# Kernel optimization log

Measured on AMD Instinct MI355X. Metric: run time of the kernel, lower is better.

## Reference

```python
import jax, jax.numpy as jnp
import numpy as np

B, L = 1, 2048
D_MODEL, N_LAYER, D_INNER = 768, 2, 1536
D_STATE, DT_RANK, D_CONV, OUT_DIM = 16, 48, 4, 128


def setup_inputs() -> dict:
    key = jax.random.key(0)
    ks = jax.random.split(key, 10)
    s = 0.02
    p = {}
    p["x"] = jax.random.normal(ks[0], (B, L, D_MODEL), jnp.float32)
    # stacked per-layer parameters, leading dim = N_LAYER
    p["in_proj_w"] = jax.random.normal(ks[1], (N_LAYER, 2 * D_INNER, D_MODEL), jnp.float32) * s
    p["conv_w"] = jax.random.normal(ks[2], (N_LAYER, D_INNER, D_CONV), jnp.float32) * s
    p["conv_b"] = jnp.zeros((N_LAYER, D_INNER), jnp.float32)
    p["x_proj_w"] = jax.random.normal(ks[3], (N_LAYER, DT_RANK + 2 * D_STATE, D_INNER), jnp.float32) * s
    p["dt_proj_w"] = jax.random.normal(ks[4], (N_LAYER, D_INNER, DT_RANK), jnp.float32) * s
    p["dt_proj_b"] = jax.random.normal(ks[5], (N_LAYER, D_INNER), jnp.float32) * s
    A = jnp.tile(jnp.arange(1, D_STATE + 1, dtype=jnp.float32)[None, :], (D_INNER, 1))
    p["A_log"] = jnp.tile(jnp.log(A)[None], (N_LAYER, 1, 1))
    p["D"] = jnp.ones((N_LAYER, D_INNER), jnp.float32)
    p["out_proj_w"] = jax.random.normal(ks[6], (N_LAYER, D_MODEL, D_INNER), jnp.float32) * s
    p["norm_w"] = jnp.ones((N_LAYER, D_MODEL), jnp.float32)
    p["norm_f_w"] = jnp.ones((D_MODEL,), jnp.float32)
    p["head_w"] = jax.random.normal(ks[7], (OUT_DIM, D_MODEL), jnp.float32) * s
    return p


def rmsnorm(x, w, eps=1e-5):
    return x * jax.lax.rsqrt(jnp.mean(x * x, -1, keepdims=True) + eps) * w


def selective_scan(u, delta, A, Bm, Cm, Dv):
    # u, delta: (b,l,d); A: (d,n); Bm, Cm: (b,l,n); Dv: (d,)
    dA = jnp.exp(jnp.einsum('bld,dn->bldn', delta, A))       # discretized A
    dBu = jnp.einsum('bld,bln->bldn', delta * u, Bm)          # discretized B*u

    def step(s, inp):
        dA_t, dBu_t, C_t = inp                               # (b,d,n),(b,d,n),(b,n)
        s = dA_t * s + dBu_t
        y = jnp.einsum('bdn,bn->bd', s, C_t)
        return s, y

    s0 = jnp.zeros((u.shape[0], u.shape[2], A.shape[1]), u.dtype)
    _, ys = jax.lax.scan(step, s0, (dA.transpose(1, 0, 2, 3), dBu.transpose(1, 0, 2, 3), Cm.transpose(1, 0, 2)))
    y = ys.transpose(1, 0, 2)                                # (b,l,d)
    return y + u * Dv


def mamba_block(x, w):
    xr = jnp.einsum('bld,ed->ble', x, w['in_proj_w'])        # (b,l,2*d_inner)
    xin, res = jnp.split(xr, 2, axis=-1)
    # causal depthwise conv1d
    xc = jax.lax.conv_general_dilated(
        xin.transpose(0, 2, 1), w['conv_w'][:, None, :],
        window_strides=(1,), padding=[(D_CONV - 1, 0)],
        dimension_numbers=('NCH', 'OIH', 'NCH'),
        feature_group_count=D_INNER)
    xc = (xc + w['conv_b'][None, :, None]).transpose(0, 2, 1)
    xc = jax.nn.silu(xc)
    # SSM
    A = -jnp.exp(w['A_log'])                                 # (d_inner, d_state)
    proj = jnp.einsum('bld,ed->ble', xc, w['x_proj_w'])
    delta, Bm, Cm = jnp.split(proj, [DT_RANK, DT_RANK + D_STATE], axis=-1)
    delta = jax.nn.softplus(jnp.einsum('blr,dr->bld', delta, w['dt_proj_w']) + w['dt_proj_b'])
    y = selective_scan(xc, delta, A, Bm, Cm, w['D'])
    y = y * jax.nn.silu(res)
    return jnp.einsum('bld,ed->ble', y, w['out_proj_w'])


def reference(x, in_proj_w, conv_w, conv_b, x_proj_w, dt_proj_w, dt_proj_b,
              A_log, D, out_proj_w, norm_w, norm_f_w, head_w):
    stacked = dict(in_proj_w=in_proj_w, conv_w=conv_w, conv_b=conv_b,
                   x_proj_w=x_proj_w, dt_proj_w=dt_proj_w, dt_proj_b=dt_proj_b,
                   A_log=A_log, D=D, out_proj_w=out_proj_w)
    for i in range(N_LAYER):
        w = {k: v[i] for k, v in stacked.items()}
        x = x + mamba_block(rmsnorm(x, norm_w[i]), w)        # pre-norm residual block
    x = rmsnorm(x, norm_f_w)
    return jnp.einsum('bld,od->blo', x, head_w)              # lm_head (no bias)
```

## Files before the change

### kernel.cpp

```cpp
#include <hip/hip_runtime.h>
#include <hip/hip_bf16.h>
#include <stdint.h>

#define LSEQ 2048
#define DM 768
#define DI 1536
#define NCH 128
#define CHK 16

typedef __bf16 bf16;
typedef short short8 __attribute__((ext_vector_type(8)));
typedef float floatx4 __attribute__((ext_vector_type(4)));
typedef bf16 bf16x8 __attribute__((ext_vector_type(8)));

__device__ inline float silu_f(float x){ return x / (1.f + __expf(-x)); }

__device__ __forceinline__ void g2l16(const bf16* g, bf16* l){
  __builtin_amdgcn_global_load_lds(
      (const __attribute__((address_space(1))) void*)g,
      (__attribute__((address_space(3))) void*)l, 16, 0, 0);
}

__device__ inline int bf16_flag(const void* dvv){
  return (*(const unsigned*)dvv == 0x3F803F80u) ? 1 : 0;
}

__device__ inline float ldin(const void* p, long i, int f){
  return f ? (float)((const bf16*)p)[i] : ((const float*)p)[i];
}

__device__ __forceinline__ void ld8(const void* src, long i, int f, float* o){
  if(f){
    bf16x8 v = *(const bf16x8*)((const bf16*)src + i);
    #pragma unroll
    for(int k = 0; k < 8; k++) o[k] = (float)v[k];
  } else {
    float4 a = ((const float4*)src)[i >> 2];
    float4 b = ((const float4*)src)[(i >> 2) + 1];
    o[0]=a.x; o[1]=a.y; o[2]=a.z; o[3]=a.w; o[4]=b.x; o[5]=b.y; o[6]=b.z; o[7]=b.w;
  }
}
__device__ __forceinline__ void st8_bf(bf16* dst, long i, const float* o){
  bf16x8 v;
  #pragma unroll
  for(int k = 0; k < 8; k++) v[k] = (bf16)o[k];
  *(bf16x8*)(dst + i) = v;
}
__device__ __forceinline__ void st8_f32(float* dst, long i, const float* o){
  ((float4*)dst)[i >> 2]       = make_float4(o[0], o[1], o[2], o[3]);
  ((float4*)dst)[(i >> 2) + 1] = make_float4(o[4], o[5], o[6], o[7]);
}

#define NB_INW  2304
#define NB_OUTW 1152
#define NB_HW   48
#define NB_X    768
#define NB_ALOG 24
#define NB_XPW  192
#define NB_DTW  96
#define NB_SM   12
#define NB_TOT  (NB_INW+NB_OUTW+NB_HW+NB_X+NB_ALOG+NB_XPW+NB_DTW+NB_SM)

__global__ __launch_bounds__(256) void k_canon(const void* x_, const void* inw_,
    const void* cw_, const void* cb_, const void* xpw_, const void* dtw_,
    const void* dtb_, const void* dvv_, const void* alog_, const void* outw_,
    const void* nw_, const void* nfw_, const void* hw_,
    float* x0, bf16* inw, float* cw, float* cb, bf16* xpw, bf16* dtw, float* dtb,
    float* alog, float* dv, bf16* outw, float* nw, float* nfw, bf16* hw){
  int f = bf16_flag(dvv_);
  int b = blockIdx.x;
  int t = threadIdx.x;
  float o[8];
  if(b < NB_INW + NB_OUTW + NB_HW){
    const void* src; bf16* dst; long off;
    if(b < NB_INW){ src = inw_; dst = inw; off = (long)b*2048; }
    else if(b < NB_INW + NB_OUTW){ src = outw_; dst = outw; off = (long)(b - NB_INW)*2048; }
    else { src = hw_; dst = hw; off = (long)(b - NB_INW - NB_OUTW)*2048; }
    long i = off + t*8;
    if(f){ *(bf16x8*)(dst + i) = *(const bf16x8*)((const bf16*)src + i); }
    else { ld8(src, i, 0, o); st8_bf(dst, i, o); }
    return;
  }
  b -= NB_INW + NB_OUTW + NB_HW;
  if(b < NB_X + NB_ALOG){
    const void* src; float* dst; long off;
    if(b < NB_X){ src = x_; dst = x0; off = (long)b*2048; }
    else { src = alog_; dst = alog; off = (long)(b - NB_X)*2048; }
    long i = off + t*8;
    ld8(src, i, f, o);
    st8_f32(dst, i, o);
    return;
  }
  b -= NB_X + NB_ALOG;
  if(b < NB_XPW){
    long j = (long)b*2048 + t*8;
    int layer = (int)(j / (128*DI));
    int rem = (int)(j % (128*DI));
    int r = rem / DI, c = rem % DI;
    if(r < 80){
      ld8(xpw_, ((long)layer*80 + r)*DI + c, f, o);
    } else {
      for(int k = 0; k < 8; k++) o[k] = 0.f;
    }
    st8_bf(xpw, j, o);
    return;
  }
  b -= NB_XPW;
  if(b < NB_DTW){
    long j = (long)b*2048 + t*8;
    int layer = (int)(j / (DI*64));
    int rem = (int)(j % (DI*64));
    int r = rem / 64, c = rem % 64;
    if(c < 48){
      ld8(dtw_, ((long)layer*DI + r)*48 + c, f, o);
    } else {
      for(int k = 0; k < 8; k++) o[k] = 0.f;
    }
    st8_bf(dtw, j, o);
    return;
  }
  b -= NB_DTW;
  for(int idx = b*256 + t; idx < 23808; idx += NB_SM*256){
    int j = idx;
    if(j < 12288){ cw[j] = ldin(cw_, j, f); continue; } j -= 12288;
    if(j < 3072){ cb[j] = ldin(cb_, j, f); continue; } j -= 3072;
    if(j < 3072){ dtb[j] = ldin(dtb_, j, f); continue; } j -= 3072;
    if(j < 3072){ dv[j] = ldin(dvv_, j, f); continue; } j -= 3072;
    if(j < 1536){ nw[j] = ldin(nw_, j, f); continue; } j -= 1536;
    nfw[j] = ldin(nfw_, j, f);
  }
}

__global__ __launch_bounds__(256) void k_rmsnorm(const float* __restrict__ x,
    const float* __restrict__ w, bf16* __restrict__ out){
  int row = blockIdx.x;
  const float* xr = x + row*DM;
  int t = threadIdx.x;
  float v0 = xr[t], v1 = xr[t+256], v2 = xr[t+512];
  float ss = v0*v0 + v1*v1 + v2*v2;
  #pragma unroll
  for(int o = 32; o; o >>= 1) ss += __shfl_down(ss, o, 64);
  __shared__ float red[4];
  int lane = t & 63, wid = t >> 6;
  if(lane == 0) red[wid] = ss;
  __syncthreads();
  ss = red[0] + red[1] + red[2] + red[3];
  float rs = rsqrtf(ss / DM + 1e-5f);
  out[row*DM + t]       = (bf16)(v0 * rs * w[t]);
  out[row*DM + t + 256] = (bf16)(v1 * rs * w[t+256]);
  out[row*DM + t + 512] = (bf16)(v2 * rs * w[t+512]);
}

template<int SPLITK, int MODE>
__global__ __launch_bounds__(256) void k_gemm(
    const bf16* __restrict__ A, const bf16* __restrict__ B, void* Cv,
    int K, int ldc, const float* __restrict__ aux){
  __shared__ bf16 sA[64*32];
  __shared__ bf16 sB[128*32];
  int bm0 = blockIdx.y*64, bn0 = blockIdx.x*128;
  int tid = threadIdx.x;
  int lane = tid & 63, wid = tid >> 6;
  int wn = wid*32;
  int quad = lane >> 4, lr = lane & 15;
  const int klen = K / SPLITK;
  const int kbeg = (SPLITK > 1) ? blockIdx.z * klen : 0;
  const bf16* Ag = A + (size_t)(bm0 + (tid>>2))*K + kbeg + (tid&3)*8;
  const bf16* Bg = B + (size_t)(bn0 + (tid>>2))*K + kbeg + (tid&3)*8;
  floatx4 acc[4][2] = {};
  for(int k0 = 0; k0 < klen; k0 += 32){
    __syncthreads();
    g2l16(Ag, sA + tid*8);
    g2l16(Bg, sB + tid*8);
    g2l16(Bg + 64*K, sB + 2048 + tid*8);
    __syncthreads();
    short8 af[4], bf_[2];
    #pragma unroll
    for(int i = 0; i < 4; i++)
      af[i]  = *(const short8*)(sA + (i*16 + lr)*32 + quad*8);
    #pragma unroll
    for(int j = 0; j < 2; j++)
      bf_[j] = *(const short8*)(sB + (wn + j*16 + lr)*32 + quad*8);
    #pragma unroll
    for(int i = 0; i < 4; i++)
      #pragma unroll
      for(int j = 0; j < 2; j++)
        acc[i][j] = __builtin_amdgcn_mfma_f32_16x16x32_bf16(af[i], bf_[j], acc[i][j], 0, 0, 0);
    Ag += 32; Bg += 32;
  }
  float* Cf = (float*)Cv + ((MODE == 5) ? (size_t)blockIdx.z * LSEQ * ldc : 0);
  bf16* Cb = (bf16*)Cv;
  #pragma unroll
  for(int i = 0; i < 4; i++){
    #pragma unroll
    for(int j = 0; j < 2; j++){
      #pragma unroll
      for(int r = 0; r < 4; r++){
        int grow = bm0 + i*16 + quad*4 + r;
        int gcol = bn0 + wn + j*16 + lr;
        float v = acc[i][j][r];
        if(MODE == 0){
          Cb[(size_t)grow*ldc + gcol] = (bf16)v;
        } else if(MODE == 1){
          v += aux[gcol];
          v = fmaxf(v, 0.f) + log1pf(__expf(-fabsf(v)));
          Cb[(size_t)grow*ldc + gcol] = (bf16)v;
        } else {
          Cf[(size_t)grow*ldc + gcol] = v;
        }
      }
    }
  }
  (void)aux;
}

__global__ __launch_bounds__(256) void k_epi_xproj(const float* __restrict__ part,
    float* __restrict__ proj, bf16* __restrict__ dtin){
  int idx = blockIdx.x*256 + threadIdx.x;
  float s = 0.f;
  #pragma unroll
  for(int z = 0; z < 8; z++) s += part[(size_t)z*LSEQ*128 + idx];
  int row = idx >> 7, col = idx & 127;
  if(col < 80) proj[row*80 + col] = s;
  if(col < 64) dtin[row*64 + col] = (col < 48) ? (bf16)s : (bf16)0.f;
}

__global__ __launch_bounds__(256) void k_epi_out_norm(const float* __restrict__ part,
    const float* __restrict__ resid, const float* __restrict__ w,
    float* __restrict__ xws, bf16* __restrict__ xn){
  int row = blockIdx.x;
  int t = threadIdx.x;
  float v[3]; float ss = 0.f;
  #pragma unroll
  for(int k = 0; k < 3; k++){
    long i = (long)row*DM + t + k*256;
    float s = part[i] + part[(long)LSEQ*DM + i] + resid[i];
    xws[i] = s; v[k] = s; ss += s*s;
  }
  #pragma unroll
  for(int o = 32; o; o >>= 1) ss += __shfl_down(ss, o, 64);
  __shared__ float red[4];
  if((t & 63) == 0) red[t >> 6] = ss;
  __syncthreads();
  ss = red[0] + red[1] + red[2] + red[3];
  float rs = rsqrtf(ss / DM + 1e-5f);
  #pragma unroll
  for(int k = 0; k < 3; k++){
    int col = t + k*256;
    xn[(long)row*DM + col] = (bf16)(v[k] * rs * w[col]);
  }
}

__global__ __launch_bounds__(256) void k_epi_head(const float* __restrict__ part,
    const void* dvv, void* out){
  int idx = blockIdx.x*256 + threadIdx.x;
  const int N = LSEQ*128;
  float s = part[idx] + part[N+idx] + part[2*N+idx] + part[3*N+idx];
  if(bf16_flag(dvv)) ((bf16*)out)[idx] = (bf16)s;
  else               ((float*)out)[idx] = s;
}

__global__ __launch_bounds__(256) void k_conv(const bf16* __restrict__ xr,
    const float* __restrict__ cw, const float* __restrict__ cb,
    bf16* __restrict__ xcb){
  int d = blockIdx.x*256 + threadIdx.x;
  int l0 = blockIdx.y*16;
  float w0 = cw[d*4+0], w1 = cw[d*4+1], w2 = cw[d*4+2], w3 = cw[d*4+3];
  float bias = cb[d];
  float xm3 = (l0 >= 3) ? (float)xr[(l0-3)*(2*DI) + d] : 0.f;
  float xm2 = (l0 >= 2) ? (float)xr[(l0-2)*(2*DI) + d] : 0.f;
  float xm1 = (l0 >= 1) ? (float)xr[(l0-1)*(2*DI) + d] : 0.f;
  #pragma unroll
  for(int tl = 0; tl < 16; tl++){
    int l = l0 + tl;
    float xc = (float)xr[l*(2*DI) + d];
    float acc = bias + xm3*w0 + xm2*w1 + xm1*w2 + xc*w3;
    xcb[l*DI + d] = (bf16)silu_f(acc);
    xm3 = xm2; xm2 = xm1; xm1 = xc;
  }
}

__global__ __launch_bounds__(256) void k_scan1(
    const bf16* __restrict__ delta, const bf16* __restrict__ u,
    const float* __restrict__ proj, const float* __restrict__ alog,
    float* __restrict__ Aprod, float* __restrict__ Bsum){
  int d = blockIdx.y*256 + threadIdx.x;
  int c = blockIdx.x;
  __shared__ float Bl[CHK*16];
  {
    int t = threadIdx.x >> 4, n = threadIdx.x & 15;
    Bl[threadIdx.x] = proj[(c*CHK + t)*80 + 48 + n];
  }
  __syncthreads();
  const float L2E = 1.44269504f;
  float An2[16], ap[16], s[16];
  #pragma unroll
  for(int n = 0; n < 16; n++){ An2[n] = -__expf(alog[d*16+n]) * L2E; ap[n] = 1.f; s[n] = 0.f; }
  int t0 = c*CHK;
  float dt = (float)delta[t0*DI + d];
  float uu = (float)u[t0*DI + d];
  #pragma unroll
  for(int tl = 0; tl < CHK; tl++){
    float dtn = 0.f, un = 0.f;
    if(tl + 1 < CHK){
      dtn = (float)delta[(t0+tl+1)*DI + d];
      un = (float)u[(t0+tl+1)*DI + d];
    }
    float du = dt * uu;
    #pragma unroll
    for(int n = 0; n < 16; n++){
      float e = exp2f(dt * An2[n]);
      s[n] = e*s[n] + du*Bl[tl*16+n];
      ap[n] *= e;
    }
    dt = dtn; uu = un;
  }
  int base = (c*DI + d)*16;
  #pragma unroll
  for(int n = 0; n < 16; n++){ Aprod[base+n] = ap[n]; Bsum[base+n] = s[n]; }
}

__global__ __launch_bounds__(256) void k_scan2(const float* __restrict__ Aprod,
    const float* __restrict__ Bsum, float* __restrict__ Sinit){
  int idx = blockIdx.x*256 + threadIdx.x;
  const int STR = DI*16;
  float s = 0.f;
  for(int c0 = 0; c0 < NCH; c0 += 8){
    float a[8], b[8];
    #pragma unroll
    for(int j = 0; j < 8; j++){
      a[j] = Aprod[(size_t)(c0+j)*STR + idx];
      b[j] = Bsum [(size_t)(c0+j)*STR + idx];
    }
    #pragma unroll
    for(int j = 0; j < 8; j++){
      Sinit[(size_t)(c0+j)*STR + idx] = s;
      s = a[j]*s + b[j];
    }
  }
}

__global__ __launch_bounds__(256) void k_scan3(
    const bf16* __restrict__ delta, const bf16* __restrict__ u,
    const float* __restrict__ proj, const float* __restrict__ alog,
    const float* __restrict__ dvp, const float* __restrict__ Sinit,
    const bf16* __restrict__ xr, bf16* __restrict__ ybar){
  int d = blockIdx.y*256 + threadIdx.x;
  int c = blockIdx.x;
  __shared__ float Bl[CHK*16], Cl[CHK*16];
  {
    int t = threadIdx.x >> 4, n = threadIdx.x & 15;
    Bl[threadIdx.x] = proj[(c*CHK + t)*80 + 48 + n];
    Cl[threadIdx.x] = proj[(c*CHK + t)*80 + 64 + n];
  }
  __syncthreads();
  const float L2E = 1.44269504f;
  float An2[16], s[16];
  #pragma unroll
  for(int n = 0; n < 16; n++) An2[n] = -__expf(alog[d*16+n]) * L2E;
  int base = (c*DI + d)*16;
  #pragma unroll
  for(int n = 0; n < 16; n++) s[n] = Sinit[base+n];
  float Dd = dvp[d];
  int t0 = c*CHK;
  float dt = (float)delta[t0*DI + d];
  float uu = (float)u[t0*DI + d];
  float res = (float)xr[t0*(2*DI) + DI + d];
  #pragma unroll
  for(int tl = 0; tl < CHK; tl++){
    float dtn = 0.f, un = 0.f, rn = 0.f;
    if(tl + 1 < CHK){
      dtn = (float)delta[(t0+tl+1)*DI + d];
      un = (float)u[(t0+tl+1)*DI + d];
      rn = (float)xr[(t0+tl+1)*(2*DI) + DI + d];
    }
    float du = dt * uu;
    float y = 0.f;
    #pragma unroll
    for(int n = 0; n < 16; n++){
      float e = exp2f(dt * An2[n]);
      s[n] = e*s[n] + du*Bl[tl*16+n];
      y += s[n]*Cl[tl*16+n];
    }
    y += uu * Dd;
    ybar[(t0+tl)*DI + d] = (bf16)(y * silu_f(res));
    dt = dtn; uu = un; res = rn;
  }
}

extern "C" void kernel_launch(void* const* d_in, const int* in_sizes, int n_in,
                              void* d_out, int out_size, void* d_ws, size_t ws_size,
                              hipStream_t stream){
  const void* x_   = d_in[0];
  const void* inw_ = d_in[1];
  const void* cw_  = d_in[2];
  const void* cb_  = d_in[3];
  const void* xpw_ = d_in[4];
  const void* dtw_ = d_in[5];
  const void* dtb_ = d_in[6];
  const void* alog_= d_in[7];
  const void* dvv_ = d_in[8];
  const void* outw_= d_in[9];
  const void* nw_  = d_in[10];
  const void* nfw_ = d_in[11];
  const void* hw_  = d_in[12];

  char* p = (char*)d_ws;
  auto alloc = [&](size_t n){ char* r = p; p += (n + 255) & ~(size_t)255; return r; };
  float* x0  = (float*)alloc((size_t)LSEQ*DM*4);
  bf16* inw  = (bf16*)alloc((size_t)2*2*DI*DM*2);
  float* cw  = (float*)alloc((size_t)2*DI*4*4);
  float* cb  = (float*)alloc((size_t)2*DI*4);
  bf16* xpw  = (bf16*)alloc((size_t)2*128*DI*2);
  bf16* dtw  = (bf16*)alloc((size_t)2*DI*64*2);
  float* dtb = (float*)alloc((size_t)2*DI*4);
  float* alog= (float*)alloc((size_t)2*DI*16*4);
  float* dv  = (float*)alloc((size_t)2*DI*4);
  bf16* outw = (bf16*)alloc((size_t)2*DM*DI*2);
  float* nw  = (float*)alloc((size_t)2*DM*4);
  float* nfw = (float*)alloc((size_t)DM*4);
  bf16* hw   = (bf16*)alloc((size_t)128*DM*2);
  bf16* xn   = (bf16*)alloc((size_t)LSEQ*DM*2);
  bf16* xr   = (bf16*)alloc((size_t)LSEQ*2*DI*2);
  bf16* xcb  = (bf16*)alloc((size_t)LSEQ*DI*2);
  float* proj= (float*)alloc((size_t)LSEQ*80*4);
  bf16* dtin = (bf16*)alloc((size_t)LSEQ*64*2);
  bf16* delta= (bf16*)alloc((size_t)LSEQ*DI*2);
  float* Aprod=(float*)alloc((size_t)NCH*DI*16*4);
  float* Bsum =(float*)alloc((size_t)NCH*DI*16*4);
  bf16* ybar = (bf16*)alloc((size_t)LSEQ*DI*2);
  float* xws = (float*)alloc((size_t)LSEQ*DM*4);
  float* part = (float*)alloc((size_t)2*LSEQ*DM*4);
  float* Sinit = part;

  k_canon<<<NB_TOT, 256, 0, stream>>>(x_, inw_, cw_, cb_, xpw_, dtw_, dtb_, dvv_,
      alog_, outw_, nw_, nfw_, hw_,
      x0, inw, cw, cb, xpw, dtw, dtb, alog, dv, outw, nw, nfw, hw);

  k_rmsnorm<<<LSEQ, 256, 0, stream>>>(x0, nw, xn);
  const float* xcur = x0;
  for(int i = 0; i < 2; i++){
    k_gemm<1,0><<<dim3(2*DI/128, LSEQ/64), 256, 0, stream>>>(
        xn, inw + (size_t)i*2*DI*DM, xr, DM, 2*DI, nullptr);
    k_conv<<<dim3(DI/256, LSEQ/16), 256, 0, stream>>>(xr, cw + i*DI*4, cb + i*DI, xcb);
    k_gemm<8,5><<<dim3(1, LSEQ/64, 8), 256, 0, stream>>>(
        xcb, xpw + (size_t)i*128*DI, part, DI, 128, nullptr);
    k_epi_xproj<<<LSEQ*128/256, 256, 0, stream>>>(part, proj, dtin);
    k_gemm<1,1><<<dim3(DI/128, LSEQ/64), 256, 0, stream>>>(
        dtin, dtw + (size_t)i*DI*64, delta, 64, DI, dtb + i*DI);
    k_scan1<<<dim3(NCH, DI/256), 256, 0, stream>>>(delta, xcb, proj, alog + i*DI*16, Aprod, Bsum);
    k_scan2<<<DI*16/256, 256, 0, stream>>>(Aprod, Bsum, Sinit);
    k_scan3<<<dim3(NCH, DI/256), 256, 0, stream>>>(delta, xcb, proj, alog + i*DI*16,
        dv + i*DI, Sinit, xr, ybar);
    k_gemm<2,5><<<dim3(DM/128, LSEQ/64, 2), 256, 0, stream>>>(
        ybar, outw + (size_t)i*DM*DI, part, DI, DM, nullptr);
    k_epi_out_norm<<<LSEQ, 256, 0, stream>>>(part, xcur,
        (i == 0) ? (nw + DM) : nfw, xws, xn);
    xcur = xws;
  }
  k_gemm<4,5><<<dim3(1, LSEQ/64, 4), 256, 0, stream>>>(
      xn, hw, part, DM, 128, nullptr);
  k_epi_head<<<LSEQ*128/256, 256, 0, stream>>>(part, dvv_, d_out);

  (void)in_sizes; (void)n_in; (void)out_size; (void)ws_size;
}
```

Baseline: 408.2 us.

## Fuse x_proj split-K reduction with dt_proj softplus; preload scan inputs

Replaces the x_proj epilogue kernel and the separate MFMA dt_proj GEMM with one kernel per row. It reduces the split-K partials, keeps the 48-wide dt row in shared memory, computes dt_proj with scalar FMAs and softplus, and writes delta. This removes one launch and the dtin round trip, but moves the small K=48 GEMM from matrix cores onto vector ALUs. Separately, the scan kernels now load all 16 delta and u values for a chunk up front rather than prefetching one step ahead, which raises register use.

```diff
diff --git a/kernel.cpp b/kernel.cpp
--- a/kernel.cpp
+++ b/kernel.cpp
@@ -154,7 +154,7 @@
 template<int SPLITK, int MODE>
 __global__ __launch_bounds__(256) void k_gemm(
     const bf16* __restrict__ A, const bf16* __restrict__ B, void* Cv,
-    int K, int ldc, const float* __restrict__ aux){
+    int K, int ldc){
   __shared__ bf16 sA[64*32];
   __shared__ bf16 sB[128*32];
   int bm0 = blockIdx.y*64, bn0 = blockIdx.x*128;
@@ -198,30 +198,44 @@
         int grow = bm0 + i*16 + quad*4 + r;
         int gcol = bn0 + wn + j*16 + lr;
         float v = acc[i][j][r];
-        if(MODE == 0){
-          Cb[(size_t)grow*ldc + gcol] = (bf16)v;
-        } else if(MODE == 1){
-          v += aux[gcol];
-          v = fmaxf(v, 0.f) + log1pf(__expf(-fabsf(v)));
-          Cb[(size_t)grow*ldc + gcol] = (bf16)v;
-        } else {
-          Cf[(size_t)grow*ldc + gcol] = v;
-        }
+        if(MODE == 0) Cb[(size_t)grow*ldc + gcol] = (bf16)v;
+        else          Cf[(size_t)grow*ldc + gcol] = v;
       }
     }
   }
-  (void)aux;
-}
-
-__global__ __launch_bounds__(256) void k_epi_xproj(const float* __restrict__ part,
-    float* __restrict__ proj, bf16* __restrict__ dtin){
-  int idx = blockIdx.x*256 + threadIdx.x;
-  float s = 0.f;
-  #pragma unroll
-  for(int z = 0; z < 8; z++) s += part[(size_t)z*LSEQ*128 + idx];
-  int row = idx >> 7, col = idx & 127;
-  if(col < 80) proj[row*80 + col] = s;
-  if(col < 64) dtin[row*64 + col] = (col < 48) ? (bf16)s : (bf16)0.f;
+}
+
+__global__ __launch_bounds__(256) void k_xproj_dt(
+    const float* __restrict__ part, const bf16* __restrict__ dtw,
+    const float* __restrict__ dtb, float* __restrict__ proj,
+    bf16* __restrict__ delta){
+  int l = blockIdx.x;
+  int t = threadIdx.x;
+  __shared__ float prow[80];
+  if(t < 128){
+    float s = 0.f;
+    #pragma unroll
+    for(int z = 0; z < 8; z++) s += part[(size_t)z*LSEQ*128 + (size_t)l*128 + t];
+    if(t < 80){ prow[t] = s; proj[(size_t)l*80 + t] = s; }
+  }
+  __syncthreads();
+  float a[48];
+  #pragma unroll
+  for(int j = 0; j < 48; j++) a[j] = prow[j];
+  #pragma unroll
+  for(int k = 0; k < 6; k++){
+    int n = t + k*256;
+    const bf16* w = dtw + (size_t)n*64;
+    float acc = dtb[n];
+    #pragma unroll
+    for(int j0 = 0; j0 < 48; j0 += 8){
+      bf16x8 wv = *(const bf16x8*)(w + j0);
+      #pragma unroll
+      for(int j = 0; j < 8; j++) acc += a[j0+j]*(float)wv[j];
+    }
+    acc = fmaxf(acc, 0.f) + log1pf(__expf(-fabsf(acc)));
+    delta[(size_t)l*DI + n] = (bf16)acc;
+  }
 }
 
 __global__ __launch_bounds__(256) void k_epi_out_norm(const float* __restrict__ part,
@@ -291,28 +305,27 @@
     Bl[threadIdx.x] = proj[(c*CHK + t)*80 + 48 + n];
   }
   __syncthreads();
+  int t0 = c*CHK;
+  float dts[CHK], us[CHK];
+  #pragma unroll
+  for(int tl = 0; tl < CHK; tl++){
+    dts[tl] = (float)delta[(size_t)(t0+tl)*DI + d];
+    us[tl]  = (float)u[(size_t)(t0+tl)*DI + d];
+  }
   const float L2E = 1.44269504f;
   float An2[16], ap[16], s[16];
   #pragma unroll
   for(int n = 0; n < 16; n++){ An2[n] = -__expf(alog[d*16+n]) * L2E; ap[n] = 1.f; s[n] = 0.f; }
-  int t0 = c*CHK;
-  float dt = (float)delta[t0*DI + d];
-  float uu = (float)u[t0*DI + d];
   #pragma unroll
   for(int tl = 0; tl < CHK; tl++){
-    float dtn = 0.f, un = 0.f;
-    if(tl + 1 < CHK){
-      dtn = (float)delta[(t0+tl+1)*DI + d];
-      un = (float)u[(t0+tl+1)*DI + d];
-    }
-    float du = dt * uu;
+    float dt = dts[tl];
+    float du = dt * us[tl];
     #pragma unroll
     for(int n = 0; n < 16; n++){
       float e = exp2f(dt * An2[n]);
       s[n] = e*s[n] + du*Bl[tl*16+n];
       ap[n] *= e;
     }
-    dt = dtn; uu = un;
   }
   int base = (c*DI + d)*16;
   #pragma unroll
@@ -353,6 +366,13 @@
     Cl[threadIdx.x] = proj[(c*CHK + t)*80 + 64 + n];
   }
   __syncthreads();
+  int t0 = c*CHK;
+  float dts[CHK], us[CHK];
+  #pragma unroll
+  for(int tl = 0; tl < CHK; tl++){
+    dts[tl] = (float)delta[(size_t)(t0+tl)*DI + d];
+    us[tl]  = (float)u[(size_t)(t0+tl)*DI + d];
+  }
   const float L2E = 1.44269504f;
   float An2[16], s[16];
   #pragma unroll
@@ -361,18 +381,12 @@
   #pragma unroll
   for(int n = 0; n < 16; n++) s[n] = Sinit[base+n];
   float Dd = dvp[d];
-  int t0 = c*CHK;
-  float dt = (float)delta[t0*DI + d];
-  float uu = (float)u[t0*DI + d];
-  float res = (float)xr[t0*(2*DI) + DI + d];
+  float res = (float)xr[(size_t)t0*(2*DI) + DI + d];
   #pragma unroll
   for(int tl = 0; tl < CHK; tl++){
-    float dtn = 0.f, un = 0.f, rn = 0.f;
-    if(tl + 1 < CHK){
-      dtn = (float)delta[(t0+tl+1)*DI + d];
-      un = (float)u[(t0+tl+1)*DI + d];
-      rn = (float)xr[(t0+tl+1)*(2*DI) + DI + d];
-    }
+    float rn = (tl + 1 < CHK) ? (float)xr[(size_t)(t0+tl+1)*(2*DI) + DI + d] : 0.f;
+    float dt = dts[tl];
+    float uu = us[tl];
     float du = dt * uu;
     float y = 0.f;
     #pragma unroll
@@ -382,8 +396,8 @@
       y += s[n]*Cl[tl*16+n];
     }
     y += uu * Dd;
-    ybar[(t0+tl)*DI + d] = (bf16)(y * silu_f(res));
-    dt = dtn; uu = un; res = rn;
+    ybar[(size_t)(t0+tl)*DI + d] = (bf16)(y * silu_f(res));
+    res = rn;
   }
 }
 
@@ -423,7 +437,6 @@
   bf16* xr   = (bf16*)alloc((size_t)LSEQ*2*DI*2);
   bf16* xcb  = (bf16*)alloc((size_t)LSEQ*DI*2);
   float* proj= (float*)alloc((size_t)LSEQ*80*4);
-  bf16* dtin = (bf16*)alloc((size_t)LSEQ*64*2);
   bf16* delta= (bf16*)alloc((size_t)LSEQ*DI*2);
   float* Aprod=(float*)alloc((size_t)NCH*DI*16*4);
   float* Bsum =(float*)alloc((size_t)NCH*DI*16*4);
@@ -440,25 +453,24 @@
   const float* xcur = x0;
   for(int i = 0; i < 2; i++){
     k_gemm<1,0><<<dim3(2*DI/128, LSEQ/64), 256, 0, stream>>>(
-        xn, inw + (size_t)i*2*DI*DM, xr, DM, 2*DI, nullptr);
+        xn, inw + (size_t)i*2*DI*DM, xr, DM, 2*DI);
     k_conv<<<dim3(DI/256, LSEQ/16), 256, 0, stream>>>(xr, cw + i*DI*4, cb + i*DI, xcb);
     k_gemm<8,5><<<dim3(1, LSEQ/64, 8), 256, 0, stream>>>(
-        xcb, xpw + (size_t)i*128*DI, part, DI, 128, nullptr);
-    k_epi_xproj<<<LSEQ*128/256, 256, 0, stream>>>(part, proj, dtin);
-    k_gemm<1,1><<<dim3(DI/128, LSEQ/64), 256, 0, stream>>>(
-        dtin, dtw + (size_t)i*DI*64, delta, 64, DI, dtb + i*DI);
+        xcb, xpw + (size_t)i*128*DI, part, DI, 128);
+    k_xproj_dt<<<LSEQ, 256, 0, stream>>>(part, dtw + (size_t)i*DI*64,
+        dtb + i*DI, proj, delta);
     k_scan1<<<dim3(NCH, DI/256), 256, 0, stream>>>(delta, xcb, proj, alog + i*DI*16, Aprod, Bsum);
     k_scan2<<<DI*16/256, 256, 0, stream>>>(Aprod, Bsum, Sinit);
     k_scan3<<<dim3(NCH, DI/256), 256, 0, stream>>>(delta, xcb, proj, alog + i*DI*16,
         dv + i*DI, Sinit, xr, ybar);
     k_gemm<2,5><<<dim3(DM/128, LSEQ/64, 2), 256, 0, stream>>>(
-        ybar, outw + (size_t)i*DM*DI, part, DI, DM, nullptr);
+        ybar, outw + (size_t)i*DM*DI, part, DI, DM);
     k_epi_out_norm<<<LSEQ, 256, 0, stream>>>(part, xcur,
         (i == 0) ? (nw + DM) : nfw, xws, xn);
     xcur = xws;
   }
   k_gemm<4,5><<<dim3(1, LSEQ/64, 4), 256, 0, stream>>>(
-      xn, hw, part, DM, 128, nullptr);
+      xn, hw, part, DM, 128);
   k_epi_head<<<LSEQ*128/256, 256, 0, stream>>>(part, dvv_, d_out);
 
   (void)in_sizes; (void)n_in; (void)out_size; (void)ws_size;
```

After: 483.5 us. 1.18x slower.
